# Performance work log

Hardware: AMD Instinct MI355X
Metric: run time of the kernel (lower is better)

The kernel has to match this reference:

```python
import jax, jax.numpy as jnp
import numpy as np

# dims per init_kwargs / input_specs
D = 512      # embed_dim
A = 64       # mixture_count == anchor_count
V_IN = 32000
V_OUT = 32000
B = 32
S_ENC = 1024
S_DEC = 256
EPS = 1e-6   # repo LayerNorm: a2*(x-mean)/(std+eps)+b2, unbiased std


def layer_norm(x, g, b):
    m = jnp.mean(x, axis=-1, keepdims=True)
    s = jnp.std(x, axis=-1, keepdims=True, ddof=1)
    return g * (x - m) / (s + EPS) + b


def setup_inputs() -> dict:
    key = jax.random.key(0)
    ks = jax.random.split(key, 16)
    p = lambda i, shape: jax.random.normal(ks[i], shape, dtype=jnp.float32) * 0.02
    return {
        "input_sequence": jax.random.randint(ks[0], (B, S_ENC), 0, V_IN),
        "output_sequence": jax.random.randint(ks[1], (B, S_DEC), 0, V_OUT),
        "emb_in": p(2, (V_IN, D)),
        "emb_out": p(3, (V_OUT, D)),
        "enc_key_W": p(4, (A, D)),
        "enc_Wq": p(5, (D, D)), "enc_bq": jnp.zeros((D,), jnp.float32),
        "enc_Wk": p(6, (D, D)), "enc_bk": jnp.zeros((D,), jnp.float32),
        "n1_g": jnp.ones((D,), jnp.float32), "n1_b": jnp.zeros((D,), jnp.float32),
        "dec_key_W": p(7, (A, D)),
        "rdr_Wq": p(8, (D, D)), "rdr_bq": jnp.zeros((D,), jnp.float32),
        "rdr_Wk": p(9, (D, D)), "rdr_bk": jnp.zeros((D,), jnp.float32),
        "rdr_Wv": p(10, (D, D)), "rdr_bv": jnp.zeros((D,), jnp.float32),
        "dat_Wq": p(11, (D, D)), "dat_bq": jnp.zeros((D,), jnp.float32),
        "dat_Wk": p(12, (D, D)), "dat_bk": jnp.zeros((D,), jnp.float32),
        "n2_g": jnp.ones((D,), jnp.float32), "n2_b": jnp.zeros((D,), jnp.float32),
        "n3_g": jnp.ones((D,), jnp.float32), "n3_b": jnp.zeros((D,), jnp.float32),
        "voc_W": p(13, (V_OUT, D)), "voc_b": jnp.zeros((V_OUT,), jnp.float32),
    }


def reference(input_sequence, output_sequence, emb_in, emb_out, enc_key_W,
              enc_Wq, enc_bq, enc_Wk, enc_bk, n1_g, n1_b, dec_key_W,
              rdr_Wq, rdr_bq, rdr_Wk, rdr_bk, rdr_Wv, rdr_bv,
              dat_Wq, dat_bq, dat_Wk, dat_bk, n2_g, n2_b, n3_g, n3_b,
              voc_W, voc_b):
    scale = 1.0 / jnp.sqrt(jnp.float32(D))
    x_enc = emb_in[input_sequence] * jnp.sqrt(jnp.float32(D))  # [B,S,D]
    # ---- encode: sequential anchor-gated memory scan ----
    Qa = enc_key_W @ enc_Wq.T + enc_bq                         # [A,D], step-invariant

    def enc_step(carry, xt):
        z, av = carry                                          # z [B,1,D], av [B,A,D]
        z = layer_norm(z + xt[:, None, :], n1_g, n1_b)
        k = z @ enc_Wk.T + enc_bk                              # [B,1,D]
        gate = jax.nn.sigmoid(jnp.einsum('ad,bod->bao', Qa, k) * scale)  # [B,A,1]
        av = layer_norm((1.0 - gate) * av + gate * z, n1_g, n1_b)
        return (z, av), None

    z0 = jnp.zeros((B, 1, D), jnp.float32)
    av0 = jnp.zeros((B, A, D), jnp.float32)
    (z, av), _ = jax.lax.scan(enc_step, (z0, av0), jnp.swapaxes(x_enc, 0, 1))
    # ---- decode: embedded output tokens / mover / ximg are dead code in original ----
    Kr = av @ rdr_Wk.T + rdr_bk                                # [B,A,D], constant over steps
    Vr = av @ rdr_Wv.T + rdr_bv
    Qax = dec_key_W @ dat_Wq.T + dat_bq                        # [A,D]

    def dec_step(carry, _):
        z, avx = carry
        q = z @ rdr_Wq.T + rdr_bq                              # [B,1,D]
        att = jax.nn.softmax(jnp.einsum('bod,bad->boa', q, Kr) * scale, axis=-1)
        dg2 = jnp.einsum('boa,bad->bod', att, Vr)              # [B,1,D]
        kz = z @ dat_Wk.T + dat_bk
        gate = jax.nn.sigmoid(jnp.einsum('ad,bod->bao', Qax, kz) * scale)
        avx = layer_norm((1.0 - gate) * avx + gate * z, n3_g, n3_b)
        z = layer_norm(z + dg2, n2_g, n2_b)
        return (z, avx), None

    avx0 = jnp.zeros((B, A, D), jnp.float32)
    (z, avx), _ = jax.lax.scan(dec_step, (z, avx0), None, length=S_DEC)
    logits = z @ voc_W.T + voc_b                               # [B,1,V_OUT]
    return jax.nn.log_softmax(logits, axis=-1)
```

## Files before the change

kernel.cpp:

```cpp
#include <hip/hip_runtime.h>
#include <math.h>

#define DD 512
#define AA 64
#define NB 32
#define SENC 1024
#define SDEC 256
#define VOUT 32000
#define EPSL 1e-6f
#define SCALE 0.044194173824159216f
#define SQRTD 22.627416997969522f

typedef _Float16 h2 __attribute__((ext_vector_type(2)));
typedef float f32x2 __attribute__((ext_vector_type(2)));

template<int C, int R>
__device__ __forceinline__ float dppz(float v){
  return __int_as_float(__builtin_amdgcn_update_dpp(0, __float_as_int(v), C, R, 0xf, true));
}
template<int C, int R>
__device__ __forceinline__ float dppself(float v){
  return __int_as_float(__builtin_amdgcn_update_dpp(__float_as_int(v), __float_as_int(v), C, R, 0xf, false));
}
__device__ __forceinline__ float rlane63(float v){
  return __int_as_float(__builtin_amdgcn_readlane(__float_as_int(v), 63));
}
__device__ __forceinline__ void wred2(float &a, float &b){
  a += dppz<0x111,0xf>(a); b += dppz<0x111,0xf>(b);
  a += dppz<0x112,0xf>(a); b += dppz<0x112,0xf>(b);
  a += dppz<0x114,0xf>(a); b += dppz<0x114,0xf>(b);
  a += dppz<0x118,0xf>(a); b += dppz<0x118,0xf>(b);
  a += dppz<0x142,0xa>(a); b += dppz<0x142,0xa>(b);
  a += dppz<0x143,0xc>(a); b += dppz<0x143,0xc>(b);
  a = rlane63(a); b = rlane63(b);
}
__device__ __forceinline__ float wredsum(float a){
  a += dppz<0x111,0xf>(a); a += dppz<0x112,0xf>(a);
  a += dppz<0x114,0xf>(a); a += dppz<0x118,0xf>(a);
  a += dppz<0x142,0xa>(a); a += dppz<0x143,0xc>(a);
  return rlane63(a);
}
__device__ __forceinline__ float wredmax(float a){
  a = fmaxf(a, dppself<0x111,0xf>(a));
  a = fmaxf(a, dppself<0x112,0xf>(a));
  a = fmaxf(a, dppself<0x114,0xf>(a));
  a = fmaxf(a, dppself<0x118,0xf>(a));
  a = fmaxf(a, dppself<0x142,0xa>(a));
  a = fmaxf(a, dppself<0x143,0xc>(a));
  return rlane63(a);
}
__device__ __forceinline__ unsigned int pk16(float x, float y){
  return __builtin_bit_cast(unsigned int, __builtin_amdgcn_cvt_pkrtz(x, y));
}
__device__ __forceinline__ float fd2(unsigned int a, unsigned int b, float c){
#if __has_builtin(__builtin_amdgcn_fdot2)
  return __builtin_amdgcn_fdot2(__builtin_bit_cast(h2, a), __builtin_bit_cast(h2, b), c, false);
#else
  h2 x = __builtin_bit_cast(h2, a), y = __builtin_bit_cast(h2, b);
  return c + (float)x[0]*(float)y[0] + (float)x[1]*(float)y[1];
#endif
}
__device__ __forceinline__ float frcp(float x){ float r; asm("v_rcp_f32 %0, %1" : "=v"(r) : "v"(x)); return r; }
__device__ __forceinline__ float fsqrt_f(float x){ float r; asm("v_sqrt_f32 %0, %1" : "=v"(r) : "v"(x)); return r; }
__device__ __forceinline__ f32x2 pkfma(f32x2 a, f32x2 b, f32x2 c){
  return __builtin_elementwise_fma(a, b, c);
}

__global__ void __launch_bounds__(512) qa_kernel(const float* __restrict__ keyW,
    const float* __restrict__ Wq, const float* __restrict__ bq, float* __restrict__ Qa){
  int a = blockIdx.x, i = threadIdx.x;
  __shared__ float key[DD];
  key[i] = keyW[a*DD + i];
  __syncthreads();
  const float4* w4 = (const float4*)(Wq + (size_t)i*DD);
  const float4* k4 = (const float4*)key;
  float s = 0.f;
  #pragma unroll 4
  for (int j = 0; j < DD/4; j++){
    float4 w = w4[j], k = k4[j];
    s = fmaf(w.x,k.x, fmaf(w.y,k.y, fmaf(w.z,k.z, fmaf(w.w,k.w, s))));
  }
  Qa[a*DD + i] = s + bq[i];
}

__global__ void __launch_bounds__(512) menc_kernel(const float* __restrict__ Qa,
    const float* __restrict__ Wk, float* __restrict__ Menc){
  int a = blockIdx.x, j = threadIdx.x;
  __shared__ float qa[DD];
  qa[j] = Qa[a*DD + j];
  __syncthreads();
  float s = 0.f;
  #pragma unroll 4
  for (int i = 0; i < DD; i++) s = fmaf(qa[i], Wk[(size_t)i*DD + j], s);
  Menc[a*DD + j] = s;
}

__global__ void __launch_bounds__(256) dotb_kernel(const float* __restrict__ X,
    const float* __restrict__ v, float* __restrict__ out){
  int m = blockIdx.x*4 + (threadIdx.x >> 6);
  int lane = threadIdx.x & 63;
  const float4* x4 = (const float4*)(X + (size_t)m*DD + lane*8);
  const float4* v4 = (const float4*)(v + lane*8);
  float4 a = x4[0], b4 = x4[1], c = v4[0], d = v4[1];
  float s = a.x*c.x;
  s = fmaf(a.y,c.y, s); s = fmaf(a.z,c.z, s); s = fmaf(a.w,c.w, s);
  s = fmaf(b4.x,d.x, s); s = fmaf(b4.y,d.y, s); s = fmaf(b4.z,d.z, s); s = fmaf(b4.w,d.w, s);
  s = wredsum(s);
  if (lane == 0) out[m] = s;
}

__global__ void __launch_bounds__(512) flag_kernel(const float* __restrict__ g,
    const float* __restrict__ b, int* __restrict__ flag){
  __shared__ int s;
  if (threadIdx.x == 0) s = 1;
  __syncthreads();
  bool ok = (g[threadIdx.x] == 1.0f) && (b[threadIdx.x] == 0.0f);
  if (!ok) atomicAnd(&s, 0);
  __syncthreads();
  if (threadIdx.x == 0) flag[0] = s;
}

__global__ void __launch_bounds__(256) xgather_kernel(const int* __restrict__ toks,
    const float* __restrict__ emb, float* __restrict__ X){
  int row = blockIdx.x*4 + (threadIdx.x >> 6);
  int lane = threadIdx.x & 63;
  int tok = toks[row];
  const float4* src = (const float4*)(emb + (size_t)tok*DD + lane*8);
  float4 a = src[0], b = src[1];
  a.x*=SQRTD; a.y*=SQRTD; a.z*=SQRTD; a.w*=SQRTD;
  b.x*=SQRTD; b.y*=SQRTD; b.z*=SQRTD; b.w*=SQRTD;
  float4* dst = (float4*)(X + (size_t)row*DD + lane*8);
  dst[0] = a; dst[1] = b;
}

__device__ __forceinline__ void zscan_fast(float* __restrict__ XZ, float* __restrict__ ZSQ){
  int b = blockIdx.x, lane = threadIdx.x;
  int bd = lane*8;
  f32x2 z0 = {0.f,0.f}, z1 = {0.f,0.f}, z2 = {0.f,0.f}, z3 = {0.f,0.f};
  float* xp = XZ + (size_t)b*SENC*DD + bd;
  float2* sqp = (float2*)ZSQ + (size_t)b*SENC;
  float4 xa0 = *(const float4*)(xp       ), xb0 = *(const float4*)(xp        + 4);
  float4 xa1 = *(const float4*)(xp + DD  ), xb1 = *(const float4*)(xp + DD   + 4);
  float4 xa2 = *(const float4*)(xp + 2*DD), xb2 = *(const float4*)(xp + 2*DD + 4);
  float4 xa3 = *(const float4*)(xp + 3*DD), xb3 = *(const float4*)(xp + 3*DD + 4);
  for (int t = 0; t < SENC; t += 4){
#define ZFSTEP(XA, XB, OFS, PFO, TI) {                                             \
    f32x2 y0 = z0 + f32x2{XA.x, XA.y}, y1 = z1 + f32x2{XA.z, XA.w};                \
    f32x2 y2 = z2 + f32x2{XB.x, XB.y}, y3 = z3 + f32x2{XB.z, XB.w};                \
    f32x2 t01 = y0 + y1, t23 = y2 + y3, tv = t01 + t23;                            \
    float s = tv.x + tv.y;                                                         \
    f32x2 q0 = y0*y0, q1 = y1*y1, q2 = y2*y2, q3 = y3*y3;                          \
    f32x2 q01 = q0 + q1, q23 = q2 + q3, qv = q01 + q23;                            \
    float q = qv.x + qv.y;                                                         \
    wred2(s, q);                                                                   \
    float mean = s * (1.f/DD);                                                     \
    float qc2  = fmaf(mean*(-(float)DD), mean, q);                                 \
    float var  = fmaxf(qc2 * (1.f/(DD-1)), 0.f);                                   \
    float r = frcp(fsqrt_f(var) + EPSL);                                           \
    float c3 = -(r*mean);                                                          \
    f32x2 RR = {r,r}, C3 = {c3,c3};                                                \
    z0 = pkfma(RR, y0, C3); z1 = pkfma(RR, y1, C3);                                \
    z2 = pkfma(RR, y2, C3); z3 = pkfma(RR, y3, C3);                                \
    if (lane == 0){ float2 o = {0.f, qc2*r*r}; sqp[TI] = o; }                      \
    float4 o1 = {z0.x,z0.y,z1.x,z1.y}, o2 = {z2.x,z2.y,z3.x,z3.y};                 \
    *(float4*)(xp + OFS) = o1; *(float4*)(xp + OFS + 4) = o2;                      \
    XA = *(const float4*)(xp + PFO); XB = *(const float4*)(xp + PFO + 4); }
    ZFSTEP(xa0, xb0, 0,    4*DD, 0)
    ZFSTEP(xa1, xb1, DD,   5*DD, 1)
    ZFSTEP(xa2, xb2, 2*DD, 6*DD, 2)
    ZFSTEP(xa3, xb3, 3*DD, 7*DD, 3)
#undef ZFSTEP
    xp += 4*DD; sqp += 4;
  }
}

__device__ __forceinline__ void zscan_gen(float* __restrict__ XZ,
    const float* __restrict__ n1g, const float* __restrict__ n1b,
    float* __restrict__ ZSQ){
  int b = blockIdx.x, lane = threadIdx.x;
  int bd = lane*8;
  float z[8], g1[8], b1[8];
  #pragma unroll
  for (int k = 0; k < 8; k++) z[k] = 0.f;
  *(float4*)&g1[0] = *(const float4*)(n1g+bd); *(float4*)&g1[4] = *(const float4*)(n1g+bd+4);
  *(float4*)&b1[0] = *(const float4*)(n1b+bd); *(float4*)&b1[4] = *(const float4*)(n1b+bd+4);
  float* xp = XZ + (size_t)b*SENC*DD + bd;
  float2* sqp = (float2*)ZSQ + (size_t)b*SENC;
  for (int t = 0; t < SENC; t++){
    float4 xa = *(const float4*)xp, xb = *(const float4*)(xp + 4);
    float x[8] = {xa.x,xa.y,xa.z,xa.w,xb.x,xb.y,xb.z,xb.w};
    float y[8], s = 0.f, q = 0.f;
    #pragma unroll
    for (int k = 0; k < 8; k++){ y[k] = z[k] + x[k]; s += y[k]; q = fmaf(y[k], y[k], q); }
    wred2(s, q);
    float mean = s * (1.f/DD);
    float var  = fmaxf((q - (float)DD*mean*mean) * (1.f/(DD-1)), 0.f);
    float r = 1.f/(sqrtf(var) + EPSL);
    float sz = 0.f, qz = 0.f;
    #pragma unroll
    for (int k = 0; k < 8; k++){
      z[k] = fmaf(g1[k]*r, y[k]-mean, b1[k]);
      sz += z[k]; qz = fmaf(z[k], z[k], qz);
    }
    wred2(sz, qz);
    if (lane == 0){ float2 o = {sz, qz}; sqp[t] = o; }
    float4 o1 = {z[0],z[1],z[2],z[3]}, o2 = {z[4],z[5],z[6],z[7]};
    *(float4*)xp = o1; *(float4*)(xp + 4) = o2;
    xp += DD;
  }
}

__global__ void __launch_bounds__(64) zscan_kernel(float* __restrict__ XZ,
    const float* __restrict__ n1g, const float* __restrict__ n1b,
    const int* __restrict__ flag, float* __restrict__ ZSQ){
  if (flag[0]) zscan_fast(XZ, ZSQ);
  else         zscan_gen(XZ, n1g, n1b, ZSQ);
}

__global__ void __launch_bounds__(256) gates_kernel(const float* __restrict__ Zin,
    const float* __restrict__ Menc, const float* __restrict__ cenc,
    float* __restrict__ gates){
  __shared__ float As[32][64];
  __shared__ float Bs[32][64];
  int tid = threadIdx.x;
  int m0 = blockIdx.x*64;
  int ty = tid >> 4, tx = tid & 15;
  float acc[4][4] = {{0.f}};
  for (int k0 = 0; k0 < 512; k0 += 32){
    #pragma unroll
    for (int p = 0; p < 2; p++){
      int row = (tid>>3) + p*32, col = (tid&7)*4;
      float4 va = *(const float4*)(Zin + (size_t)(m0+row)*512 + k0 + col);
      As[col][row]=va.x; As[col+1][row]=va.y; As[col+2][row]=va.z; As[col+3][row]=va.w;
      float4 vb = *(const float4*)(Menc + (size_t)row*512 + k0 + col);
      Bs[col][row]=vb.x; Bs[col+1][row]=vb.y; Bs[col+2][row]=vb.z; Bs[col+3][row]=vb.w;
    }
    __syncthreads();
    #pragma unroll
    for (int kk = 0; kk < 32; kk++){
      float4 a4 = *(const float4*)&As[kk][ty*4];
      float4 b4 = *(const float4*)&Bs[kk][tx*4];
      float au[4] = {a4.x,a4.y,a4.z,a4.w}, bv[4] = {b4.x,b4.y,b4.z,b4.w};
      #pragma unroll
      for (int u = 0; u < 4; u++)
        #pragma unroll
        for (int v = 0; v < 4; v++) acc[u][v] = fmaf(au[u], bv[v], acc[u][v]);
    }
    __syncthreads();
  }
  float cv[4];
  #pragma unroll
  for (int v = 0; v < 4; v++) cv[v] = cenc[tx*4 + v];
  #pragma unroll
  for (int u = 0; u < 4; u++){
    float4 st;
    st.x = frcp(1.f + __expf(-(acc[u][0]+cv[0])*SCALE));
    st.y = frcp(1.f + __expf(-(acc[u][1]+cv[1])*SCALE));
    st.z = frcp(1.f + __expf(-(acc[u][2]+cv[2])*SCALE));
    st.w = frcp(1.f + __expf(-(acc[u][3]+cv[3])*SCALE));
    *(float4*)(gates + (size_t)(m0+ty*4+u)*AA + tx*4) = st;
  }
}

__device__ __forceinline__ void avscan_fast(const float* __restrict__ Z,
    const float* __restrict__ ZSQ, const float* __restrict__ gates,
    float* __restrict__ avout){
  int bx = blockIdx.x;
  int b = (bx & 7)*4 + ((bx >> 3) & 3);
  int a = ((bx >> 5)<<3) + (threadIdx.x >> 6);
  int lane = threadIdx.x & 63;
  int bd = lane*8;
  f32x2 av0 = {0.f,0.f}, av1 = {0.f,0.f}, av2v = {0.f,0.f}, av3 = {0.f,0.f};
  float Qav = 0.f;
  const float*  zp  = Z + (size_t)b*SENC*DD + bd;
  const float4* sp4 = (const float4*)(ZSQ + (size_t)b*SENC*2);
  const float*  gp  = gates + (size_t)b*SENC*AA + a;
  float4 zc0a = *(const float4*)zp,        zc0b = *(const float4*)(zp + 4);
  float4 zc1a = *(const float4*)(zp + DD), zc1b = *(const float4*)(zp + DD + 4);
  float4 sq01 = sp4[0];
  float g0 = gp[0], g1 = gp[AA];
  for (int t = 0; t < SENC; t += 2){
    float4 zn0a = *(const float4*)(zp + 2*DD), zn0b = *(const float4*)(zp + 2*DD + 4);
    float4 zn1a = *(const float4*)(zp + 3*DD), zn1b = *(const float4*)(zp + 3*DD + 4);
    float4 sqn = sp4[1];
    float gn0 = gp[2*AA], gn1 = gp[3*AA];
#define AVSTEP(ZA, ZB, SZT, QZT, G) {                                              \
    f32x2 z0 = {ZA.x, ZA.y}, z1 = {ZA.z, ZA.w};                                    \
    f32x2 z2 = {ZB.x, ZB.y}, z3 = {ZB.z, ZB.w};                                    \
    f32x2 p0 = av0*z0, p1 = av1*z1, p2 = av2v*z2, p3 = av3*z3;                     \
    f32x2 s01 = p0 + p1, s23 = p2 + p3, sv = s01 + s23;                            \
    float cav = wredsum(sv.x + sv.y);                                              \
    float g = (G), omg = 1.f - g;                                                  \
    float mean = (g * (1.f/DD)) * (SZT);                                           \
    float a1s = (omg*omg) * Qav;                                                   \
    float a2s = fmaf((g+g)*omg, cav, a1s);                                         \
    float Qy  = fmaf(g*g, (QZT), a2s);                                             \
    float qc2 = fmaf(mean*(-(float)DD), mean, Qy);                                 \
    float var = fmaxf(qc2 * (1.f/(DD-1)), 0.f);                                    \
    float r = frcp(fsqrt_f(var) + EPSL);                                           \
    float c1 = r*omg, c2s = r*g, c3 = -(r*mean);                                   \
    f32x2 C1 = {c1,c1}, C2 = {c2s,c2s}, C3 = {c3,c3};                              \
    av0  = pkfma(C1, av0,  pkfma(C2, z0, C3));                                     \
    av1  = pkfma(C1, av1,  pkfma(C2, z1, C3));                                     \
    av2v = pkfma(C1, av2v, pkfma(C2, z2, C3));                                     \
    av3  = pkfma(C1, av3,  pkfma(C2, z3, C3));                                     \
    Qav = qc2 * (r*r); }
    AVSTEP(zc0a, zc0b, sq01.x, sq01.y, g0)
    AVSTEP(zc1a, zc1b, sq01.z, sq01.w, g1)
#undef AVSTEP
    zc0a = zn0a; zc0b = zn0b; zc1a = zn1a; zc1b = zn1b;
    sq01 = sqn; g0 = gn0; g1 = gn1;
    zp += 2*DD; sp4 += 1; gp += 2*AA;
  }
  float* o = avout + ((size_t)(b*AA + a))*DD + bd;
  float4 o1 = {av0.x,av0.y,av1.x,av1.y}, o2 = {av2v.x,av2v.y,av3.x,av3.y};
  *(float4*)o = o1; *(float4*)(o+4) = o2;
}

__device__ __forceinline__ void avscan_gen(const float* __restrict__ Z,
    const float* __restrict__ ZSQ, const float* __restrict__ gates,
    const float* __restrict__ n1g, const float* __restrict__ n1b,
    float* __restrict__ avout){
  int bx = blockIdx.x;
  int b = (bx & 7)*4 + ((bx >> 3) & 3);
  int a = ((bx >> 5)<<3) + (threadIdx.x >> 6);
  int lane = threadIdx.x & 63;
  int bd = lane*8;
  float g1[8], b1[8], av[8];
  *(float4*)&g1[0] = *(const float4*)(n1g+bd); *(float4*)&g1[4] = *(const float4*)(n1g+bd+4);
  *(float4*)&b1[0] = *(const float4*)(n1b+bd); *(float4*)&b1[4] = *(const float4*)(n1b+bd+4);
  #pragma unroll
  for (int k = 0; k < 8; k++) av[k] = 0.f;
  float Sav = 0.f, Qav = 0.f;
  const float*  zp = Z + (size_t)b*SENC*DD + bd;
  const float2* sp = (const float2*)ZSQ + (size_t)b*SENC;
  const float*  gp = gates + (size_t)b*SENC*AA + a;
  for (int t = 0; t < SENC; t++){
    float4 za = *(const float4*)zp, zb = *(const float4*)(zp + 4);
    float z[8] = {za.x,za.y,za.z,za.w,zb.x,zb.y,zb.z,zb.w};
    float2 sq = sp[0];
    float g = gp[0];
    float cav = 0.f;
    #pragma unroll
    for (int k = 0; k < 8; k++) cav = fmaf(av[k], z[k], cav);
    cav = wredsum(cav);
    float omg = 1.f - g;
    float Sy = fmaf(g, sq.x - Sav, Sav);
    float Qy = omg*omg*Qav + 2.f*g*omg*cav + g*g*sq.y;
    float mean = Sy * (1.f/DD);
    float var  = fmaxf((Qy - (float)DD*mean*mean) * (1.f/(DD-1)), 0.f);
    float r = 1.f/(sqrtf(var) + EPSL);
    float sn = 0.f, qn = 0.f;
    #pragma unroll
    for (int k = 0; k < 8; k++){
      float y = fmaf(g, z[k]-av[k], av[k]);
      float nv = fmaf(g1[k]*r, y-mean, b1[k]);
      av[k] = nv; sn += nv; qn = fmaf(nv, nv, qn);
    }
    wred2(sn, qn);
    Sav = sn; Qav = qn;
    zp += DD; sp += 1; gp += AA;
  }
  float* o = avout + ((size_t)(b*AA + a))*DD + bd;
  float4 o1 = {av[0],av[1],av[2],av[3]}, o2 = {av[4],av[5],av[6],av[7]};
  *(float4*)o = o1; *(float4*)(o+4) = o2;
}

__global__ void __launch_bounds__(512) avscan_kernel(const float* __restrict__ Z,
    const float* __restrict__ ZSQ, const float* __restrict__ gates,
    const float* __restrict__ n1g, const float* __restrict__ n1b,
    const int* __restrict__ flag, float* __restrict__ avout){
  if (flag[0]) avscan_fast(Z, ZSQ, gates, avout);
  else         avscan_gen(Z, ZSQ, gates, n1g, n1b, avout);
}

__global__ void __launch_bounds__(256) gemm_nt_kernel(const float* __restrict__ Aa,
    const float* __restrict__ Bw, const float* __restrict__ bias,
    void* __restrict__ Cout, int mode){
  __shared__ float As[32][64];
  __shared__ float Bs[32][64];
  int tid = threadIdx.x;
  int m0 = blockIdx.x*64, n0 = blockIdx.y*64;
  int ty = tid >> 4, tx = tid & 15;
  float acc[4][4] = {{0.f}};
  for (int k0 = 0; k0 < 512; k0 += 32){
    #pragma unroll
    for (int p = 0; p < 2; p++){
      int row = (tid>>3) + p*32, col = (tid&7)*4;
      float4 va = *(const float4*)(Aa + (size_t)(m0+row)*512 + k0 + col);
      As[col][row]=va.x; As[col+1][row]=va.y; As[col+2][row]=va.z; As[col+3][row]=va.w;
      float4 vb = *(const float4*)(Bw + (size_t)(n0+row)*512 + k0 + col);
      Bs[col][row]=vb.x; Bs[col+1][row]=vb.y; Bs[col+2][row]=vb.z; Bs[col+3][row]=vb.w;
    }
    __syncthreads();
    #pragma unroll
    for (int kk = 0; kk < 32; kk++){
      float4 a4 = *(const float4*)&As[kk][ty*4];
      float4 b4 = *(const float4*)&Bs[kk][tx*4];
      float au[4] = {a4.x,a4.y,a4.z,a4.w}, bv[4] = {b4.x,b4.y,b4.z,b4.w};
      #pragma unroll
      for (int u = 0; u < 4; u++)
        #pragma unroll
        for (int v = 0; v < 4; v++) acc[u][v] = fmaf(au[u], bv[v], acc[u][v]);
    }
    __syncthreads();
  }
  float bv4[4];
  #pragma unroll
  for (int v = 0; v < 4; v++) bv4[v] = bias ? bias[n0 + tx*4 + v] : 0.f;
  if (mode == 0){
    float* C = (float*)Cout;
    #pragma unroll
    for (int u = 0; u < 4; u++){
      float4 st = {acc[u][0]+bv4[0], acc[u][1]+bv4[1], acc[u][2]+bv4[2], acc[u][3]+bv4[3]};
      *(float4*)(C + (size_t)(m0+ty*4+u)*512 + n0 + tx*4) = st;
    }
  } else {
    unsigned short* C = (unsigned short*)Cout;
    #pragma unroll
    for (int u = 0; u < 4; u++){
      int mm = m0 + ty*4 + u; int bb = mm >> 6, a2 = mm & 63;
      #pragma unroll
      for (int v = 0; v < 4; v++){
        _Float16 hv = (_Float16)(acc[u][v] + bv4[v]);
        C[((size_t)bb*512 + n0 + tx*4 + v)*64 + a2] = __builtin_bit_cast(unsigned short, hv);
      }
    }
  }
}

__global__ void __launch_bounds__(256) gemm_nn_kernel(const float* __restrict__ Aa,
    const float* __restrict__ Bw, unsigned int* __restrict__ Cout){
  __shared__ float As[32][64];
  __shared__ float Bs[32][64];
  int tid = threadIdx.x;
  int m0 = blockIdx.x*64, n0 = blockIdx.y*64;
  int ty = tid >> 4, tx = tid & 15;
  float acc[4][4] = {{0.f}};
  for (int k0 = 0; k0 < 512; k0 += 32){
    #pragma unroll
    for (int p = 0; p < 2; p++){
      int row = (tid>>3) + p*32, col = (tid&7)*4;
      float4 va = *(const float4*)(Aa + (size_t)(m0+row)*512 + k0 + col);
      As[col][row]=va.x; As[col+1][row]=va.y; As[col+2][row]=va.z; As[col+3][row]=va.w;
      int brow = (tid>>4) + p*16, bcol = (tid&15)*4;
      float4 vb = *(const float4*)(Bw + (size_t)(k0+brow)*512 + n0 + bcol);
      *(float4*)&Bs[brow][bcol] = vb;
    }
    __syncthreads();
    #pragma unroll
    for (int kk = 0; kk < 32; kk++){
      float4 a4 = *(const float4*)&As[kk][ty*4];
      float4 b4 = *(const float4*)&Bs[kk][tx*4];
      float au[4] = {a4.x,a4.y,a4.z,a4.w}, bv[4] = {b4.x,b4.y,b4.z,b4.w};
      #pragma unroll
      for (int u = 0; u < 4; u++)
        #pragma unroll
        for (int v = 0; v < 4; v++) acc[u][v] = fmaf(au[u], bv[v], acc[u][v]);
    }
    __syncthreads();
  }
  #pragma unroll
  for (int u = 0; u < 4; u++){
    uint2 st = { pk16(acc[u][0], acc[u][1]), pk16(acc[u][2], acc[u][3]) };
    *(uint2*)(Cout + (size_t)(m0+ty*4+u)*256 + (n0 + tx*4)/2) = st;
  }
}

__global__ void __launch_bounds__(256) dec_kernel(const float* __restrict__ Z,
    const unsigned int* __restrict__ Pg, const unsigned int* __restrict__ Vg,
    const float* __restrict__ cdec, const float* __restrict__ n2g,
    const float* __restrict__ n2b, float* __restrict__ zfin){
  __shared__ __align__(16) unsigned char Pl[65536];
  __shared__ __align__(16) unsigned char Vl[65536];
  __shared__ unsigned int zh[256];
  __shared__ float part[AA][4];
  __shared__ unsigned int att4h[4][32];
  __shared__ float2 red2[4];
  int b = blockIdx.x, tid = threadIdx.x;
  int lane = tid & 63, w = tid >> 6;

  const uint4* Pg4 = (const uint4*)(Pg + (size_t)b*16384);
  #pragma unroll
  for (int j = 0; j < 16; j++){
    int fb = j*1024 + tid*4;
    uint4 v = Pg4[j*256 + tid];
    int a = fb >> 8;
    int off = (fb & 255) * 4;
    *(uint4*)(Pl + a*1024 + (off ^ ((a&7)<<4))) = v;
  }
  const uint4* Vg4 = (const uint4*)(Vg + (size_t)b*16384);
  #pragma unroll
  for (int j = 0; j < 16; j++){
    int fb = j*1024 + tid*4;
    uint4 v = Vg4[j*256 + tid];
    int d = fb >> 5;
    int off = (fb & 31) * 4;
    *(uint4*)(Vl + d*128 + (off ^ (((d>>1)&7)<<4))) = v;
  }
  int d0 = tid*2;
  float2 zi = *(const float2*)(Z + ((size_t)b*SENC + SENC-1)*DD + d0);
  float z0r = zi.x, z1r = zi.y;
  zh[tid] = pk16(z0r, z1r);
  float cdv = cdec[b*AA + lane];
  float g2a = n2g[d0], g2b = n2g[d0+1], b2a = n2b[d0], b2b = n2b[d0+1];
  int pk = (lane&7)<<4;
  int vk = (tid&7)<<4;
  __syncthreads();

  for (int t = 0; t < SDEC; t++){
    float s = 0.f;
    #pragma unroll
    for (int j = 0; j < 16; j++){
      uint4 pv = *(const uint4*)(Pl + lane*1024 + ((w*256 + j*16) ^ pk));
      uint4 zv = *(const uint4*)&zh[w*64 + j*4];
      s = fd2(pv.x, zv.x, s); s = fd2(pv.y, zv.y, s);
      s = fd2(pv.z, zv.z, s); s = fd2(pv.w, zv.w, s);
    }
    part[lane][w] = s;
    __syncthreads();
    float4 pp = *(const float4*)&part[lane][0];
    float l = (pp.x + pp.y + pp.z + pp.w + cdv) * SCALE;
    float mx = wredmax(l);
    float e = __expf(l - mx);
    float se = wredsum(e);
    float attv = e * frcp(se);
    float attn = dppself<0x101,0xf>(attv);
    if ((lane & 1) == 0) att4h[w][lane>>1] = pk16(attv, attn);
    asm volatile("s_waitcnt lgkmcnt(0)" ::: "memory");
    float a0 = 0.f, a1 = 0.f;
    #pragma unroll
    for (int j = 0; j < 8; j++){
      uint4 ah = *(const uint4*)&att4h[w][j*4];
      uint4 v0 = *(const uint4*)(Vl + d0*128 + ((j*16) ^ vk));
      uint4 v1 = *(const uint4*)(Vl + (d0+1)*128 + ((j*16) ^ vk));
      a0 = fd2(v0.x, ah.x, a0); a0 = fd2(v0.y, ah.y, a0);
      a0 = fd2(v0.z, ah.z, a0); a0 = fd2(v0.w, ah.w, a0);
      a1 = fd2(v1.x, ah.x, a1); a1 = fd2(v1.y, ah.y, a1);
      a1 = fd2(v1.z, ah.z, a1); a1 = fd2(v1.w, ah.w, a1);
    }
    float y0 = z0r + a0, y1 = z1r + a1;
    float s2 = y0 + y1, q2 = fmaf(y0, y0, y1*y1);
    wred2(s2, q2);
    if (lane == 0){ float2 o = {s2, q2}; red2[w] = o; }
    __syncthreads();
    float2 rA = red2[0], rB = red2[1], rC = red2[2], rD = red2[3];
    float Sy = rA.x+rB.x+rC.x+rD.x, Qy = rA.y+rB.y+rC.y+rD.y;
    float mean = Sy * (1.f/DD);
    float var  = fmaxf((Qy - (float)DD*mean*mean) * (1.f/(DD-1)), 0.f);
    float r = frcp(fsqrt_f(var) + EPSL);
    z0r = fmaf(g2a*r, y0-mean, b2a);
    z1r = fmaf(g2b*r, y1-mean, b2b);
    zh[tid] = pk16(z0r, z1r);
    asm volatile("s_waitcnt lgkmcnt(0)" ::: "memory");
  }
  zfin[(size_t)b*DD + d0]     = z0r;
  zfin[(size_t)b*DD + d0 + 1] = z1r;
}

__global__ void __launch_bounds__(256) logits_kernel(const float* __restrict__ zfin,
    const float* __restrict__ vocW, const float* __restrict__ vocb, float* __restrict__ out){
  __shared__ float zS[NB*DD];
  int tid = threadIdx.x;
  const float4* src = (const float4*)zfin;
  float4* dst = (float4*)zS;
  #pragma unroll
  for (int i = 0; i < 16; i++) dst[tid + i*256] = src[tid + i*256];
  __syncthreads();
  int w = tid >> 6, lane = tid & 63;
  int kq = lane & 3, rp = lane >> 2;
  int r0 = blockIdx.x*128 + w*32 + rp*2, r1 = r0 + 1;
  float acc0[NB], acc1[NB];
  #pragma unroll
  for (int bq = 0; bq < NB; bq++){ acc0[bq] = 0.f; acc1[bq] = 0.f; }
  const float* w0p = vocW + (size_t)r0*DD;
  const float* w1p = vocW + (size_t)r1*DD;
  for (int ks = 0; ks < 32; ks++){
    int koff = ks*16 + kq*4;
    float4 w0 = *(const float4*)(w0p + koff);
    float4 w1 = *(const float4*)(w1p + koff);
    #pragma unroll
    for (int bq = 0; bq < NB; bq++){
      float4 z4 = *(const float4*)&zS[bq*DD + koff];
      acc0[bq] = fmaf(w0.x,z4.x, fmaf(w0.y,z4.y, fmaf(w0.z,z4.z, fmaf(w0.w,z4.w, acc0[bq]))));
      acc1[bq] = fmaf(w1.x,z4.x, fmaf(w1.y,z4.y, fmaf(w1.z,z4.z, fmaf(w1.w,z4.w, acc1[bq]))));
    }
  }
  #pragma unroll
  for (int bq = 0; bq < NB; bq++){
    acc0[bq] += dppz<0xB1,0xf>(acc0[bq]); acc0[bq] += dppz<0x4E,0xf>(acc0[bq]);
    acc1[bq] += dppz<0xB1,0xf>(acc1[bq]); acc1[bq] += dppz<0x4E,0xf>(acc1[bq]);
  }
  if (kq == 0){
    float vb0 = vocb[r0], vb1 = vocb[r1];
    #pragma unroll
    for (int bq = 0; bq < NB; bq++){
      out[(size_t)bq*VOUT + r0] = acc0[bq] + vb0;
      out[(size_t)bq*VOUT + r1] = acc1[bq] + vb1;
    }
  }
}

__global__ void __launch_bounds__(256) lsm1_kernel(const float* __restrict__ out,
    float2* __restrict__ partb){
  int b = blockIdx.x >> 3, c = blockIdx.x & 7;
  const float* row = out + (size_t)b*VOUT + c*4000;
  int tid = threadIdx.x;
  __shared__ float rm[4]; __shared__ float rs[4];
  float mx = -3.4e38f;
  for (int i = tid; i < 4000; i += 256) mx = fmaxf(mx, row[i]);
  mx = wredmax(mx);
  if ((tid & 63) == 0) rm[tid>>6] = mx;
  __syncthreads();
  mx = fmaxf(fmaxf(rm[0],rm[1]), fmaxf(rm[2],rm[3]));
  float sm = 0.f;
  for (int i = tid; i < 4000; i += 256) sm += __expf(row[i] - mx);
  sm = wredsum(sm);
  if ((tid & 63) == 0) rs[tid>>6] = sm;
  __syncthreads();
  if (tid == 0){ float2 o = {mx, rs[0]+rs[1]+rs[2]+rs[3]}; partb[blockIdx.x] = o; }
}
__global__ void __launch_bounds__(256) lsm2_kernel(float* __restrict__ out,
    const float2* __restrict__ partb){
  int b = blockIdx.x >> 3, c = blockIdx.x & 7;
  float M = -3.4e38f, S = 0.f;
  #pragma unroll
  for (int j = 0; j < 8; j++) M = fmaxf(M, partb[b*8+j].x);
  #pragma unroll
  for (int j = 0; j < 8; j++){ float2 p = partb[b*8+j]; S += p.y * __expf(p.x - M); }
  float cns = M + logf(S);
  float* row = out + (size_t)b*VOUT + c*4000;
  for (int i = threadIdx.x; i < 4000; i += 256) row[i] -= cns;
}

extern "C" void kernel_launch(void* const* d_in, const int* in_sizes, int n_in,
                              void* d_out, int out_size, void* d_ws, size_t ws_size,
                              hipStream_t stream){
  (void)in_sizes; (void)n_in; (void)out_size; (void)ws_size;
  const int*   toks      = (const int*)  d_in[0];
  const float* emb_in    = (const float*)d_in[2];
  const float* enc_key_W = (const float*)d_in[4];
  const float* enc_Wq    = (const float*)d_in[5];
  const float* enc_bq    = (const float*)d_in[6];
  const float* enc_Wk    = (const float*)d_in[7];
  const float* enc_bk    = (const float*)d_in[8];
  const float* n1g       = (const float*)d_in[9];
  const float* n1b       = (const float*)d_in[10];
  const float* rdr_Wq    = (const float*)d_in[12];
  const float* rdr_bq    = (const float*)d_in[13];
  const float* rdr_Wk    = (const float*)d_in[14];
  const float* rdr_bk    = (const float*)d_in[15];
  const float* rdr_Wv    = (const float*)d_in[16];
  const float* rdr_bv    = (const float*)d_in[17];
  const float* n2g       = (const float*)d_in[22];
  const float* n2b       = (const float*)d_in[23];
  const float* vocW      = (const float*)d_in[26];
  const float* vocb      = (const float*)d_in[27];
  float* outp = (float*)d_out;

  float* ws = (float*)d_ws;
  size_t off = 0;
  float* Z    = ws + off; off += (size_t)NB*SENC*DD + 4*DD;
  float* ZSQ  = ws + off; off += (size_t)NB*SENC*2 + 8;
  float* av   = ws + off; off += (size_t)NB*AA*DD;
  float* Kr   = ws + off; float* gates = Kr; off += (size_t)NB*AA*DD;
  unsigned int* P16 = (unsigned int*)(ws + off); off += (size_t)NB*AA*DD/2;
  unsigned int* V16 = (unsigned int*)(ws + off); off += (size_t)NB*AA*DD/2;
  float* Qa   = ws + off; off += (size_t)AA*DD;
  float* Menc = ws + off; off += (size_t)AA*DD;
  float* cenc = ws + off; off += AA;
  float* cdec = ws + off; off += (size_t)NB*AA;
  float* zfin = ws + off; off += (size_t)NB*DD;
  float2* lsp = (float2*)(ws + off); off += 512;
  int*  flag  = (int*)(ws + off); off += 1;

  qa_kernel     <<<AA, 512, 0, stream>>>(enc_key_W, enc_Wq, enc_bq, Qa);
  menc_kernel   <<<AA, 512, 0, stream>>>(Qa, enc_Wk, Menc);
  dotb_kernel   <<<AA/4, 256, 0, stream>>>(Qa, enc_bk, cenc);
  flag_kernel   <<<1, 512, 0, stream>>>(n1g, n1b, flag);
  xgather_kernel<<<NB*SENC/4, 256, 0, stream>>>(toks, emb_in, Z);
  zscan_kernel  <<<NB, 64, 0, stream>>>(Z, n1g, n1b, flag, ZSQ);
  gates_kernel  <<<NB*SENC/64, 256, 0, stream>>>(Z, Menc, cenc, gates);
  avscan_kernel <<<256, 512, 0, stream>>>(Z, ZSQ, gates, n1g, n1b, flag, av);
  gemm_nt_kernel<<<dim3(NB*AA/64, DD/64), 256, 0, stream>>>(av, rdr_Wk, rdr_bk, Kr, 0);
  gemm_nn_kernel<<<dim3(NB*AA/64, DD/64), 256, 0, stream>>>(Kr, rdr_Wq, P16);
  gemm_nt_kernel<<<dim3(NB*AA/64, DD/64), 256, 0, stream>>>(av, rdr_Wv, rdr_bv, V16, 1);
  dotb_kernel   <<<NB*AA/4, 256, 0, stream>>>(Kr, rdr_bq, cdec);
  dec_kernel    <<<NB, 256, 0, stream>>>(Z, P16, V16, cdec, n2g, n2b, zfin);
  logits_kernel <<<VOUT/128, 256, 0, stream>>>(zfin, vocW, vocb, outp);
  lsm1_kernel   <<<NB*8, 256, 0, stream>>>(outp, lsp);
  lsm2_kernel   <<<NB*8, 256, 0, stream>>>(outp, lsp);
}
```

Baseline: 1.250 ms.

## Keep decoder P and V operands in registers instead of LDS

The decoder kernel now loads each thread's slices of the per-batch P matrix and V matrix straight from global memory into registers (32 uint4 per thread) once, and drops the two 64 KB swizzled LDS buffers. The 256-step loop then reads only z and the attention weights from LDS, removing per-step LDS traffic for the large operands. The dot-product accumulations are split across several independent accumulators to shorten dependency chains. The cost is much higher VGPR use, hence launch_bounds(256,1), which risks spilling and lowers occupancy, though the kernel runs only 32 blocks.

```diff
diff --git a/kernel.cpp b/kernel.cpp
--- a/kernel.cpp
+++ b/kernel.cpp
@@ -467,60 +467,48 @@
   }
 }
 
-__global__ void __launch_bounds__(256) dec_kernel(const float* __restrict__ Z,
+__global__ void __launch_bounds__(256, 1) dec_kernel(const float* __restrict__ Z,
     const unsigned int* __restrict__ Pg, const unsigned int* __restrict__ Vg,
     const float* __restrict__ cdec, const float* __restrict__ n2g,
     const float* __restrict__ n2b, float* __restrict__ zfin){
-  __shared__ __align__(16) unsigned char Pl[65536];
-  __shared__ __align__(16) unsigned char Vl[65536];
   __shared__ unsigned int zh[256];
-  __shared__ float part[AA][4];
+  __shared__ float part[AA][5];
   __shared__ unsigned int att4h[4][32];
   __shared__ float2 red2[4];
   int b = blockIdx.x, tid = threadIdx.x;
   int lane = tid & 63, w = tid >> 6;
-
-  const uint4* Pg4 = (const uint4*)(Pg + (size_t)b*16384);
-  #pragma unroll
-  for (int j = 0; j < 16; j++){
-    int fb = j*1024 + tid*4;
-    uint4 v = Pg4[j*256 + tid];
-    int a = fb >> 8;
-    int off = (fb & 255) * 4;
-    *(uint4*)(Pl + a*1024 + (off ^ ((a&7)<<4))) = v;
-  }
-  const uint4* Vg4 = (const uint4*)(Vg + (size_t)b*16384);
-  #pragma unroll
-  for (int j = 0; j < 16; j++){
-    int fb = j*1024 + tid*4;
-    uint4 v = Vg4[j*256 + tid];
-    int d = fb >> 5;
-    int off = (fb & 31) * 4;
-    *(uint4*)(Vl + d*128 + (off ^ (((d>>1)&7)<<4))) = v;
-  }
   int d0 = tid*2;
+
+  uint4 pf[16];
+  const uint4* Pg4 = (const uint4*)(Pg + ((size_t)(b*AA + lane))*256 + w*64);
+  #pragma unroll
+  for (int j = 0; j < 16; j++) pf[j] = Pg4[j];
+  uint4 vf0[8], vf1[8];
+  const uint4* Vg40 = (const uint4*)(Vg + ((size_t)b*DD + d0)*32);
+  const uint4* Vg41 = (const uint4*)(Vg + ((size_t)b*DD + d0 + 1)*32);
+  #pragma unroll
+  for (int j = 0; j < 8; j++){ vf0[j] = Vg40[j]; vf1[j] = Vg41[j]; }
+
   float2 zi = *(const float2*)(Z + ((size_t)b*SENC + SENC-1)*DD + d0);
   float z0r = zi.x, z1r = zi.y;
   zh[tid] = pk16(z0r, z1r);
   float cdv = cdec[b*AA + lane];
   float g2a = n2g[d0], g2b = n2g[d0+1], b2a = n2b[d0], b2b = n2b[d0+1];
-  int pk = (lane&7)<<4;
-  int vk = (tid&7)<<4;
   __syncthreads();
 
   for (int t = 0; t < SDEC; t++){
-    float s = 0.f;
+    float sA[4] = {0.f,0.f,0.f,0.f};
     #pragma unroll
     for (int j = 0; j < 16; j++){
-      uint4 pv = *(const uint4*)(Pl + lane*1024 + ((w*256 + j*16) ^ pk));
       uint4 zv = *(const uint4*)&zh[w*64 + j*4];
-      s = fd2(pv.x, zv.x, s); s = fd2(pv.y, zv.y, s);
-      s = fd2(pv.z, zv.z, s); s = fd2(pv.w, zv.w, s);
-    }
-    part[lane][w] = s;
-    __syncthreads();
-    float4 pp = *(const float4*)&part[lane][0];
-    float l = (pp.x + pp.y + pp.z + pp.w + cdv) * SCALE;
+      sA[j&3] = fd2(pf[j].x, zv.x, sA[j&3]);
+      sA[j&3] = fd2(pf[j].y, zv.y, sA[j&3]);
+      sA[j&3] = fd2(pf[j].z, zv.z, sA[j&3]);
+      sA[j&3] = fd2(pf[j].w, zv.w, sA[j&3]);
+    }
+    part[lane][w] = (sA[0]+sA[1]) + (sA[2]+sA[3]);
+    __syncthreads();
+    float l = (((part[lane][0] + part[lane][1]) + (part[lane][2] + part[lane][3])) + cdv) * SCALE;
     float mx = wredmax(l);
     float e = __expf(l - mx);
     float se = wredsum(e);
@@ -528,24 +516,29 @@
     float attn = dppself<0x101,0xf>(attv);
     if ((lane & 1) == 0) att4h[w][lane>>1] = pk16(attv, attn);
     asm volatile("s_waitcnt lgkmcnt(0)" ::: "memory");
-    float a0 = 0.f, a1 = 0.f;
+    float aA0 = 0.f, aA1 = 0.f, aB0 = 0.f, aB1 = 0.f;
     #pragma unroll
     for (int j = 0; j < 8; j++){
       uint4 ah = *(const uint4*)&att4h[w][j*4];
-      uint4 v0 = *(const uint4*)(Vl + d0*128 + ((j*16) ^ vk));
-      uint4 v1 = *(const uint4*)(Vl + (d0+1)*128 + ((j*16) ^ vk));
-      a0 = fd2(v0.x, ah.x, a0); a0 = fd2(v0.y, ah.y, a0);
-      a0 = fd2(v0.z, ah.z, a0); a0 = fd2(v0.w, ah.w, a0);
-      a1 = fd2(v1.x, ah.x, a1); a1 = fd2(v1.y, ah.y, a1);
-      a1 = fd2(v1.z, ah.z, a1); a1 = fd2(v1.w, ah.w, a1);
-    }
-    float y0 = z0r + a0, y1 = z1r + a1;
+      if (j & 1){
+        aA1 = fd2(vf0[j].x, ah.x, aA1); aA1 = fd2(vf0[j].y, ah.y, aA1);
+        aA1 = fd2(vf0[j].z, ah.z, aA1); aA1 = fd2(vf0[j].w, ah.w, aA1);
+        aB1 = fd2(vf1[j].x, ah.x, aB1); aB1 = fd2(vf1[j].y, ah.y, aB1);
+        aB1 = fd2(vf1[j].z, ah.z, aB1); aB1 = fd2(vf1[j].w, ah.w, aB1);
+      } else {
+        aA0 = fd2(vf0[j].x, ah.x, aA0); aA0 = fd2(vf0[j].y, ah.y, aA0);
+        aA0 = fd2(vf0[j].z, ah.z, aA0); aA0 = fd2(vf0[j].w, ah.w, aA0);
+        aB0 = fd2(vf1[j].x, ah.x, aB0); aB0 = fd2(vf1[j].y, ah.y, aB0);
+        aB0 = fd2(vf1[j].z, ah.z, aB0); aB0 = fd2(vf1[j].w, ah.w, aB0);
+      }
+    }
+    float y0 = z0r + (aA0 + aA1), y1 = z1r + (aB0 + aB1);
     float s2 = y0 + y1, q2 = fmaf(y0, y0, y1*y1);
     wred2(s2, q2);
     if (lane == 0){ float2 o = {s2, q2}; red2[w] = o; }
     __syncthreads();
     float2 rA = red2[0], rB = red2[1], rC = red2[2], rD = red2[3];
-    float Sy = rA.x+rB.x+rC.x+rD.x, Qy = rA.y+rB.y+rC.y+rD.y;
+    float Sy = (rA.x+rB.x)+(rC.x+rD.x), Qy = (rA.y+rB.y)+(rC.y+rD.y);
     float mean = Sy * (1.f/DD);
     float var  = fmaxf((Qy - (float)DD*mean*mean) * (1.f/(DD-1)), 0.f);
     float r = frcp(fsqrt_f(var) + EPSL);
```

Result: faster. 1.199 ms (-4.1%).
